# Performance work log

Hardware: AMD Instinct MI355X
Metric: run time of the kernel (lower is better)

## Reference

```python
import jax, jax.numpy as jnp
import numpy as np
import math

NUM_HEADS = 8
WINDOW = 8  # stage=1


def _windowed_attention(q, kv, Wq, bq, Wk, bk, Wv, bv, Wo, bo):
    B, N, C = q.shape
    H = W = int(math.isqrt(N))
    nh, ws = NUM_HEADS, WINDOW
    hd = C // nh
    scale = hd ** -0.5

    qp = q @ Wq + bq   # (B, N, C)
    kp = kv @ Wk + bk
    vp = kv @ Wv + bv

    def to_windows(x):
        # (B, N, C) -> (B, nh, nWh*nWw, ws*ws, hd)
        x = x.reshape(B, H // ws, ws, W // ws, ws, nh, hd)
        x = x.transpose(0, 5, 1, 3, 2, 4, 6)  # B, nh, nWh, nWw, ws, ws, hd
        return x.reshape(B, nh, (H // ws) * (W // ws), ws * ws, hd)

    qw = to_windows(qp)
    kw = to_windows(kp)
    vw = to_windows(vp)

    attn = jnp.einsum('bhnqd,bhnkd->bhnqk', qw, kw) * scale
    attn = jax.nn.softmax(attn.astype(jnp.float32), axis=-1).astype(qw.dtype)
    ow = jnp.einsum('bhnqk,bhnkd->bhnqd', attn, vw)

    # window reverse: (B, nh, nW, ws*ws, hd) -> (B, N, C)
    ow = ow.reshape(B, nh, H // ws, W // ws, ws, ws, hd)
    ow = ow.transpose(0, 2, 4, 3, 5, 1, 6)  # B, nWh, ws, nWw, ws, nh, hd
    x = ow.reshape(B, N, C)

    return x @ Wo + bo


def setup_inputs() -> dict:
    key = jax.random.key(0)
    ks = jax.random.split(key, 7)
    B, N, C = 4, 16384, 256
    s = 1.0 / math.sqrt(C)
    return {
        'q': jax.random.normal(ks[0], (B, N, C), jnp.float32),
        'kv': jax.random.normal(ks[1], (B, N, C), jnp.float32),
        'Wq': jax.random.normal(ks[2], (C, C), jnp.float32) * s,
        'bq': jnp.zeros((C,), jnp.float32),
        'Wk': jax.random.normal(ks[3], (C, C), jnp.float32) * s,
        'bk': jnp.zeros((C,), jnp.float32),
        'Wv': jax.random.normal(ks[4], (C, C), jnp.float32) * s,
        'bv': jnp.zeros((C,), jnp.float32),
        'Wo': jax.random.normal(ks[5], (C, C), jnp.float32) * s,
        'bo': jnp.zeros((C,), jnp.float32),
    }


def reference(q, kv, Wq, bq, Wk, bk, Wv, bv, Wo, bo):
    return _windowed_attention(q, kv, Wq, bq, Wk, bk, Wv, bv, Wo, bo)
```

## Files before the change

kernel.cpp:

```cpp
#include <hip/hip_runtime.h>
#include <hip/hip_bf16.h>

typedef __bf16 bf16;
typedef __bf16 bf16x8 __attribute__((ext_vector_type(8)));
typedef float  f32x4  __attribute__((ext_vector_type(4)));

#define DEVINL __device__ __forceinline__

DEVINL void gll16(const void* g, void* l) {
  __builtin_amdgcn_global_load_lds(
      (const __attribute__((address_space(1))) unsigned int*)g,
      (__attribute__((address_space(3))) unsigned int*)l, 16, 0, 0);
}

__global__ void k_prep(const float* __restrict__ Wq, const float* __restrict__ Wk,
                       const float* __restrict__ Wv, const float* __restrict__ Wo,
                       bf16* __restrict__ packQ, bf16* __restrict__ packO) {
  const int n = threadIdx.x;
  const int k = blockIdx.x;
  const int m = blockIdx.y;
  const int kk = k & 63, iter4 = k >> 6;
  const int h = kk >> 5, kg = (kk >> 3) & 3, e = k & 7;
  if (m < 3) {
    const float* W = (m == 0) ? Wq : (m == 1) ? Wk : Wv;
    const bf16 v = (bf16)W[k * 256 + n];
    const int nglob = m * 256 + n;
    const int tile = nglob >> 7, row = nglob & 127;
    packQ[(size_t)((tile * 4 + iter4) * 1024 + h * 512 + row * 4 + kg) * 8 + e] = v;
  } else {
    const float w = Wo[k * 256 + n];
    const bf16 hi = (bf16)w;
    const bf16 v = (m == 3) ? hi : (bf16)(w - (float)hi);
    const int iter = (m - 3) * 4 + iter4;
    const int tile = n >> 7, row = n & 127;
    packO[(size_t)((tile * 8 + iter) * 1024 + h * 512 + row * 4 + kg) * 8 + e] = v;
  }
}

__global__ __launch_bounds__(256, 3) void k_qkv(
    const float* __restrict__ q, const float* __restrict__ kv,
    const bf16* __restrict__ packQ,
    const float* __restrict__ bq, const float* __restrict__ bk,
    const float* __restrict__ bvv,
    bf16* __restrict__ qp, bf16* __restrict__ kp, bf16* __restrict__ vp) {
  __shared__ __align__(16) bf16 As[2][128 * 32];
  __shared__ __align__(16) bf16 Bs[2][128 * 32];

  const int g = blockIdx.x, xcd = g & 7, s = g >> 3;
  const int nb = s % 6, mh = s / 6;
  const int m0 = (mh * 8 + xcd) * 128;
  const float* A = (nb < 2) ? q : kv;

  const int tid = threadIdx.x, lane = tid & 63, wave = tid >> 6;
  const int mw = (wave >> 1) * 64, nw = (wave & 1) * 64;
  const int lm = lane & 15, lq = lane >> 4;

  f32x4 acc[4][4];
#pragma unroll
  for (int a = 0; a < 4; ++a)
#pragma unroll
    for (int b = 0; b < 4; ++b) acc[a][b] = (f32x4)0.0f;

  const int rowA = tid >> 1;
  const int hA = tid & 1;
  const bf16* pbase = packQ + (size_t)nb * 4 * 8192;

  for (int i = 0; i < 4; ++i) {
    const bf16* pit = pbase + i * 8192;
#pragma unroll
    for (int u = 0; u < 4; ++u) {
      const int c = u * 256 + tid;
      bf16* dst = (u < 2) ? &Bs[0][c * 8] : &Bs[1][(c - 512) * 8];
      gll16(pit + c * 8, dst);
    }
    const float* srcA = A + (size_t)(m0 + rowA) * 256 + i * 64 + hA * 32;
    bf16* dstA = &As[hA][rowA * 32];
#pragma unroll
    for (int half = 0; half < 2; ++half) {
      const float4 f0 = *(const float4*)(srcA + half * 16 + 0);
      const float4 f1 = *(const float4*)(srcA + half * 16 + 4);
      const float4 f2 = *(const float4*)(srcA + half * 16 + 8);
      const float4 f3 = *(const float4*)(srcA + half * 16 + 12);
      bf16x8 b0, b1;
      b0[0] = (bf16)f0.x; b0[1] = (bf16)f0.y; b0[2] = (bf16)f0.z; b0[3] = (bf16)f0.w;
      b0[4] = (bf16)f1.x; b0[5] = (bf16)f1.y; b0[6] = (bf16)f1.z; b0[7] = (bf16)f1.w;
      b1[0] = (bf16)f2.x; b1[1] = (bf16)f2.y; b1[2] = (bf16)f2.z; b1[3] = (bf16)f2.w;
      b1[4] = (bf16)f3.x; b1[5] = (bf16)f3.y; b1[6] = (bf16)f3.z; b1[7] = (bf16)f3.w;
      *(bf16x8*)&dstA[half * 16] = b0;
      *(bf16x8*)&dstA[half * 16 + 8] = b1;
    }
    __syncthreads();
#pragma unroll
    for (int ks = 0; ks < 2; ++ks) {
      bf16x8 av[4], bvf[4];
#pragma unroll
      for (int t = 0; t < 4; ++t)
        av[t] = *(const bf16x8*)&As[ks][(mw + t * 16 + lm) * 32 + lq * 8];
#pragma unroll
      for (int t = 0; t < 4; ++t)
        bvf[t] = *(const bf16x8*)&Bs[ks][(nw + t * 16 + lm) * 32 + lq * 8];
#pragma unroll
      for (int a = 0; a < 4; ++a)
#pragma unroll
        for (int b = 0; b < 4; ++b)
          acc[a][b] = __builtin_amdgcn_mfma_f32_16x16x32_bf16(av[a], bvf[b], acc[a][b], 0, 0, 0);
    }
    __syncthreads();
  }

#pragma unroll
  for (int a = 0; a < 4; ++a)
#pragma unroll
    for (int b = 0; b < 4; ++b) {
      const int nglob = nb * 128 + nw + b * 16 + lm;
      bf16* op; const float* bp; int nc;
      if (nglob < 256)      { op = qp; nc = nglob;       bp = bq; }
      else if (nglob < 512) { op = kp; nc = nglob - 256; bp = bk; }
      else                  { op = vp; nc = nglob - 512; bp = bvv; }
      const float bval = bp[nc];
#pragma unroll
      for (int r = 0; r < 4; ++r) {
        const int mg = m0 + mw + a * 16 + lq * 4 + r;
        op[(size_t)mg * 256 + nc] = (bf16)(acc[a][b][r] + bval);
      }
    }
}

__global__ __launch_bounds__(256, 3) void k_oproj(
    const bf16* __restrict__ ao, const bf16* __restrict__ packO,
    const float* __restrict__ bo, float* __restrict__ out) {
  __shared__ __align__(16) bf16 As[2][128 * 32];
  __shared__ __align__(16) bf16 Bs[2][128 * 32];

  const int g = blockIdx.x, xcd = g & 7, s = g >> 3;
  const int nb = s & 1, mh = s >> 1;
  const int m0 = (mh * 8 + xcd) * 128;

  const int tid = threadIdx.x, lane = tid & 63, wave = tid >> 6;
  const int mw = (wave >> 1) * 64, nw = (wave & 1) * 64;
  const int lm = lane & 15, lq = lane >> 4;

  f32x4 acc[4][4];
#pragma unroll
  for (int a = 0; a < 4; ++a)
#pragma unroll
    for (int b = 0; b < 4; ++b) acc[a][b] = (f32x4)0.0f;

  const bf16* pbase = packO + (size_t)nb * 8 * 8192;

  for (int i = 0; i < 8; ++i) {
    const int kA = (i & 3) * 64;
#pragma unroll
    for (int u = 0; u < 4; ++u) {
      const int c = u * 256 + tid;
      const int h = c >> 9, r2 = c & 511;
      const int row = r2 >> 2, kg = c & 3;
      bf16* dstB = (u < 2) ? &Bs[0][c * 8] : &Bs[1][(c - 512) * 8];
      gll16(pbase + (size_t)i * 8192 + c * 8, dstB);
      bf16* dstA = (u < 2) ? &As[0][r2 * 8] : &As[1][r2 * 8];
      gll16(ao + (size_t)(m0 + row) * 256 + kA + h * 32 + kg * 8, dstA);
    }
    __syncthreads();
#pragma unroll
    for (int ks = 0; ks < 2; ++ks) {
      bf16x8 av[4], bvf[4];
#pragma unroll
      for (int t = 0; t < 4; ++t)
        av[t] = *(const bf16x8*)&As[ks][(mw + t * 16 + lm) * 32 + lq * 8];
#pragma unroll
      for (int t = 0; t < 4; ++t)
        bvf[t] = *(const bf16x8*)&Bs[ks][(nw + t * 16 + lm) * 32 + lq * 8];
#pragma unroll
      for (int a = 0; a < 4; ++a)
#pragma unroll
        for (int b = 0; b < 4; ++b)
          acc[a][b] = __builtin_amdgcn_mfma_f32_16x16x32_bf16(av[a], bvf[b], acc[a][b], 0, 0, 0);
    }
    __syncthreads();
  }

#pragma unroll
  for (int a = 0; a < 4; ++a)
#pragma unroll
    for (int b = 0; b < 4; ++b) {
      const int nglob = nb * 128 + nw + b * 16 + lm;
      const float bval = bo[nglob];
#pragma unroll
      for (int r = 0; r < 4; ++r) {
        const int mg = m0 + mw + a * 16 + lq * 4 + r;
        out[(size_t)mg * 256 + nglob] = acc[a][b][r] + bval;
      }
    }
}

__global__ __launch_bounds__(256) void k_attn(
    const bf16* __restrict__ qp, const bf16* __restrict__ kp,
    const bf16* __restrict__ vp, bf16* __restrict__ ao) {
  __shared__ __align__(16) bf16 smem[3 * 64 * 136];
  bf16* Qs = smem;
  bf16* Ks = smem + 64 * 136;
  bf16* Vs = smem + 2 * 64 * 136;
  bf16* Ps = smem;
  bf16* Os = Vs;

  const int tid = threadIdx.x;
  const int lane = tid & 63;
  const int hl = tid >> 6;
  const int bw = blockIdx.x;
  const int b = bw >> 8;
  const int w = bw & 255;
  const int wy = w >> 4, wx = w & 15;
  const int ch0 = blockIdx.y * 128;

#pragma unroll
  for (int i = 0; i < 4; ++i) {
    const int c = i * 256 + tid;
    const int t = c >> 4;
    const int off = (c & 15) * 8;
    const int ty = t >> 3, tx = t & 7;
    const size_t gr = ((size_t)(b * 128 + wy * 8 + ty)) * 128 + wx * 8 + tx;
    const size_t gi = gr * 256 + ch0 + off;
    const int li = t * 136 + off;
    *(uint4*)&Qs[li] = *(const uint4*)&qp[gi];
    *(uint4*)&Ks[li] = *(const uint4*)&kp[gi];
    *(uint4*)&Vs[li] = *(const uint4*)&vp[gi];
  }
  __syncthreads();

  const int chh = hl * 32;
  const int lm = lane & 15;
  const int lq = lane >> 4;

  bf16x8 qa[4], kb[4];
#pragma unroll
  for (int t = 0; t < 4; ++t)
    qa[t] = *(const bf16x8*)&Qs[(t * 16 + lm) * 136 + chh + lq * 8];
#pragma unroll
  for (int t = 0; t < 4; ++t)
    kb[t] = *(const bf16x8*)&Ks[(t * 16 + lm) * 136 + chh + lq * 8];

  f32x4 s[4][4];
#pragma unroll
  for (int i = 0; i < 4; ++i)
#pragma unroll
    for (int j = 0; j < 4; ++j) s[i][j] = (f32x4)0.0f;
#pragma unroll
  for (int i = 0; i < 4; ++i)
#pragma unroll
    for (int j = 0; j < 4; ++j)
      s[i][j] = __builtin_amdgcn_mfma_f32_16x16x32_bf16(qa[i], kb[j], s[i][j], 0, 0, 0);

  const float scale = 0.17677669529663687f;
  float rl[4][4];
#pragma unroll
  for (int mt = 0; mt < 4; ++mt) {
#pragma unroll
    for (int r = 0; r < 4; ++r) {
      float mx = fmaxf(fmaxf(s[mt][0][r], s[mt][1][r]), fmaxf(s[mt][2][r], s[mt][3][r]));
      mx = fmaxf(mx, __shfl_xor(mx, 1));
      mx = fmaxf(mx, __shfl_xor(mx, 2));
      mx = fmaxf(mx, __shfl_xor(mx, 4));
      mx = fmaxf(mx, __shfl_xor(mx, 8));
      float sum = 0.f;
#pragma unroll
      for (int nt = 0; nt < 4; ++nt) {
        const float p = __expf((s[mt][nt][r] - mx) * scale);
        s[mt][nt][r] = p;
        sum += p;
      }
      sum += __shfl_xor(sum, 1);
      sum += __shfl_xor(sum, 2);
      sum += __shfl_xor(sum, 4);
      sum += __shfl_xor(sum, 8);
      rl[mt][r] = 1.0f / sum;
    }
  }

  __syncthreads();

  bf16* Ph = Ps + hl * 4096;
#pragma unroll
  for (int mt = 0; mt < 4; ++mt)
#pragma unroll
    for (int nt = 0; nt < 4; ++nt)
#pragma unroll
      for (int r = 0; r < 4; ++r) {
        const int qrow = mt * 16 + lq * 4 + r;
        const int kcol = nt * 16 + lm;
        Ph[qrow * 64 + (((kcol >> 3) ^ (qrow & 7)) << 3) + (kcol & 7)] = (bf16)s[mt][nt][r];
      }

  f32x4 o[4][2];
#pragma unroll
  for (int i = 0; i < 4; ++i) { o[i][0] = (f32x4)0.0f; o[i][1] = (f32x4)0.0f; }
#pragma unroll
  for (int ks = 0; ks < 2; ++ks) {
    bf16x8 pa[4];
#pragma unroll
    for (int mt = 0; mt < 4; ++mt) {
      const int qrow = mt * 16 + lm;
      const int gsel = ks * 4 + lq;
      pa[mt] = *(const bf16x8*)&Ph[qrow * 64 + ((gsel ^ (qrow & 7)) << 3)];
    }
    bf16x8 vbf[2];
#pragma unroll
    for (int ntd = 0; ntd < 2; ++ntd) {
      const int d = ntd * 16 + lm;
      bf16x8 tv;
#pragma unroll
      for (int j = 0; j < 8; ++j)
        tv[j] = Vs[(ks * 32 + lq * 8 + j) * 136 + chh + d];
      vbf[ntd] = tv;
    }
#pragma unroll
    for (int mt = 0; mt < 4; ++mt)
#pragma unroll
      for (int ntd = 0; ntd < 2; ++ntd)
        o[mt][ntd] = __builtin_amdgcn_mfma_f32_16x16x32_bf16(pa[mt], vbf[ntd], o[mt][ntd], 0, 0, 0);
  }

  __syncthreads();

#pragma unroll
  for (int mt = 0; mt < 4; ++mt)
#pragma unroll
    for (int ntd = 0; ntd < 2; ++ntd)
#pragma unroll
      for (int r = 0; r < 4; ++r) {
        const int qrow = mt * 16 + lq * 4 + r;
        const int d = ntd * 16 + lm;
        Os[qrow * 136 + chh + d] = (bf16)(o[mt][ntd][r] * rl[mt][r]);
      }
  __syncthreads();

#pragma unroll
  for (int i = 0; i < 4; ++i) {
    const int c = i * 256 + tid;
    const int t = c >> 4;
    const int off = (c & 15) * 8;
    const int ty = t >> 3, tx = t & 7;
    const size_t gr = ((size_t)(b * 128 + wy * 8 + ty)) * 128 + wx * 8 + tx;
    *(uint4*)&ao[gr * 256 + ch0 + off] = *(const uint4*)&Os[t * 136 + off];
  }
}

extern "C" void kernel_launch(void* const* d_in, const int* in_sizes, int n_in,
                              void* d_out, int out_size, void* d_ws, size_t ws_size,
                              hipStream_t stream) {
  const float* q  = (const float*)d_in[0];
  const float* kv = (const float*)d_in[1];
  const float* Wq = (const float*)d_in[2];
  const float* bq = (const float*)d_in[3];
  const float* Wk = (const float*)d_in[4];
  const float* bk = (const float*)d_in[5];
  const float* Wv = (const float*)d_in[6];
  const float* bv = (const float*)d_in[7];
  const float* Wo = (const float*)d_in[8];
  const float* bo = (const float*)d_in[9];
  float* out = (float*)d_out;

  char* ws = (char*)d_ws;
  bf16* packQ = (bf16*)(ws + 0);
  bf16* packO = (bf16*)(ws + 393216);
  const size_t PLANE = (size_t)65536 * 256 * 2;
  bf16* qp = (bf16*)(ws + 1048576);
  bf16* kp = (bf16*)(ws + 1048576 + PLANE);
  bf16* vp = (bf16*)(ws + 1048576 + 2 * PLANE);
  bf16* ao = (bf16*)(ws + 1048576 + 3 * PLANE);
  if (ws_size < 1048576 + 4 * PLANE) return;

  k_prep<<<dim3(256, 5), 256, 0, stream>>>(Wq, Wk, Wv, Wo, packQ, packO);
  k_qkv<<<3072, 256, 0, stream>>>(q, kv, packQ, bq, bk, bv, qp, kp, vp);
  k_attn<<<dim3(1024, 2), 256, 0, stream>>>(qp, kp, vp, ao);
  k_oproj<<<1024, 256, 0, stream>>>(ao, packO, bo, out);
}
```

Before: 302.1 us.

## Double-buffer QKV GEMM B tiles, load A directly into registers, swizzle LDS

The QKV projection kernel now reads the fp32 activation rows straight from global memory into registers, converts them to bf16 there and feeds them to MFMA, so the A tile no longer goes through LDS. The weight tiles are double-buffered in LDS with prefetch of the next iteration, which drops one barrier per iteration. The packed weight layout gets an XOR swizzle on the k-group to reduce LDS bank conflicts. Wave tiling changes from 2x2 (64x64) to 4x1 (32x128). The cost is more accumulator and prefetch registers, and each wave reads the weight tile separately.

Result: faster. 296.2 us (-2.0%).

```diff
diff --git a/kernel.cpp b/kernel.cpp
--- a/kernel.cpp
+++ b/kernel.cpp
@@ -26,7 +26,8 @@
     const bf16 v = (bf16)W[k * 256 + n];
     const int nglob = m * 256 + n;
     const int tile = nglob >> 7, row = nglob & 127;
-    packQ[(size_t)((tile * 4 + iter4) * 1024 + h * 512 + row * 4 + kg) * 8 + e] = v;
+    const int kgs = kg ^ ((row >> 1) & 3);
+    packQ[(size_t)((tile * 4 + iter4) * 1024 + h * 512 + row * 4 + kgs) * 8 + e] = v;
   } else {
     const float w = Wo[k * 256 + n];
     const bf16 hi = (bf16)w;
@@ -43,8 +44,7 @@
     const float* __restrict__ bq, const float* __restrict__ bk,
     const float* __restrict__ bvv,
     bf16* __restrict__ qp, bf16* __restrict__ kp, bf16* __restrict__ vp) {
-  __shared__ __align__(16) bf16 As[2][128 * 32];
-  __shared__ __align__(16) bf16 Bs[2][128 * 32];
+  __shared__ __align__(16) bf16 Bs[2][2][128 * 32];
 
   const int g = blockIdx.x, xcd = g & 7, s = g >> 3;
   const int nb = s % 6, mh = s / 6;
@@ -52,76 +52,92 @@
   const float* A = (nb < 2) ? q : kv;
 
   const int tid = threadIdx.x, lane = tid & 63, wave = tid >> 6;
-  const int mw = (wave >> 1) * 64, nw = (wave & 1) * 64;
   const int lm = lane & 15, lq = lane >> 4;
-
-  f32x4 acc[4][4];
-#pragma unroll
-  for (int a = 0; a < 4; ++a)
-#pragma unroll
-    for (int b = 0; b < 4; ++b) acc[a][b] = (f32x4)0.0f;
-
-  const int rowA = tid >> 1;
-  const int hA = tid & 1;
+  const int swzlq = lq ^ ((lm >> 1) & 3);
+  const int mw = wave * 32;
+
+  f32x4 acc[2][8];
+#pragma unroll
+  for (int t = 0; t < 2; ++t)
+#pragma unroll
+    for (int nf = 0; nf < 8; ++nf) acc[t][nf] = (f32x4)0.0f;
+
   const bf16* pbase = packQ + (size_t)nb * 4 * 8192;
-
-  for (int i = 0; i < 4; ++i) {
-    const bf16* pit = pbase + i * 8192;
+  const float* arow0 = A + (size_t)(m0 + mw + lm) * 256 + lq * 8;
+  const float* arow1 = arow0 + (size_t)16 * 256;
+
+  float4 ar[2][2][2];
+
+  auto stageB = [&](int it, int buf) {
+    const bf16* pit = pbase + it * 8192;
 #pragma unroll
     for (int u = 0; u < 4; ++u) {
       const int c = u * 256 + tid;
-      bf16* dst = (u < 2) ? &Bs[0][c * 8] : &Bs[1][(c - 512) * 8];
+      bf16* dst = (u < 2) ? &Bs[buf][0][c * 8] : &Bs[buf][1][(c - 512) * 8];
       gll16(pit + c * 8, dst);
     }
-    const float* srcA = A + (size_t)(m0 + rowA) * 256 + i * 64 + hA * 32;
-    bf16* dstA = &As[hA][rowA * 32];
-#pragma unroll
-    for (int half = 0; half < 2; ++half) {
-      const float4 f0 = *(const float4*)(srcA + half * 16 + 0);
-      const float4 f1 = *(const float4*)(srcA + half * 16 + 4);
-      const float4 f2 = *(const float4*)(srcA + half * 16 + 8);
-      const float4 f3 = *(const float4*)(srcA + half * 16 + 12);
-      bf16x8 b0, b1;
-      b0[0] = (bf16)f0.x; b0[1] = (bf16)f0.y; b0[2] = (bf16)f0.z; b0[3] = (bf16)f0.w;
-      b0[4] = (bf16)f1.x; b0[5] = (bf16)f1.y; b0[6] = (bf16)f1.z; b0[7] = (bf16)f1.w;
-      b1[0] = (bf16)f2.x; b1[1] = (bf16)f2.y; b1[2] = (bf16)f2.z; b1[3] = (bf16)f2.w;
-      b1[4] = (bf16)f3.x; b1[5] = (bf16)f3.y; b1[6] = (bf16)f3.z; b1[7] = (bf16)f3.w;
-      *(bf16x8*)&dstA[half * 16] = b0;
-      *(bf16x8*)&dstA[half * 16 + 8] = b1;
-    }
-    __syncthreads();
+  };
+  auto loadA = [&](int it) {
+#pragma unroll
+    for (int t = 0; t < 2; ++t)
+#pragma unroll
+      for (int ks = 0; ks < 2; ++ks) {
+        const float* p = (t == 0 ? arow0 : arow1) + it * 64 + ks * 32;
+        ar[t][ks][0] = *(const float4*)(p);
+        ar[t][ks][1] = *(const float4*)(p + 4);
+      }
+  };
+
+  stageB(0, 0);
+  loadA(0);
+  __syncthreads();
+
+#pragma unroll
+  for (int i = 0; i < 4; ++i) {
+    const int cur = i & 1;
+    if (i < 3) stageB(i + 1, cur ^ 1);
+
+    bf16x8 av[2][2];
+#pragma unroll
+    for (int t = 0; t < 2; ++t)
+#pragma unroll
+      for (int ks = 0; ks < 2; ++ks) {
+        const float4 f0 = ar[t][ks][0], f1 = ar[t][ks][1];
+        bf16x8 v;
+        v[0] = (bf16)f0.x; v[1] = (bf16)f0.y; v[2] = (bf16)f0.z; v[3] = (bf16)f0.w;
+        v[4] = (bf16)f1.x; v[5] = (bf16)f1.y; v[6] = (bf16)f1.z; v[7] = (bf16)f1.w;
+        av[t][ks] = v;
+      }
+    if (i < 3) loadA(i + 1);
+
 #pragma unroll
     for (int ks = 0; ks < 2; ++ks) {
-      bf16x8 av[4], bvf[4];
-#pragma unroll
-      for (int t = 0; t < 4; ++t)
-        av[t] = *(const bf16x8*)&As[ks][(mw + t * 16 + lm) * 32 + lq * 8];
-#pragma unroll
-      for (int t = 0; t < 4; ++t)
-        bvf[t] = *(const bf16x8*)&Bs[ks][(nw + t * 16 + lm) * 32 + lq * 8];
-#pragma unroll
-      for (int a = 0; a < 4; ++a)
-#pragma unroll
-        for (int b = 0; b < 4; ++b)
-          acc[a][b] = __builtin_amdgcn_mfma_f32_16x16x32_bf16(av[a], bvf[b], acc[a][b], 0, 0, 0);
-    }
-    __syncthreads();
-  }
-
-#pragma unroll
-  for (int a = 0; a < 4; ++a)
-#pragma unroll
-    for (int b = 0; b < 4; ++b) {
-      const int nglob = nb * 128 + nw + b * 16 + lm;
-      bf16* op; const float* bp; int nc;
-      if (nglob < 256)      { op = qp; nc = nglob;       bp = bq; }
-      else if (nglob < 512) { op = kp; nc = nglob - 256; bp = bk; }
-      else                  { op = vp; nc = nglob - 512; bp = bvv; }
+      bf16x8 bvf[8];
+#pragma unroll
+      for (int nf = 0; nf < 8; ++nf)
+        bvf[nf] = *(const bf16x8*)&Bs[cur][ks][(nf * 16 + lm) * 32 + swzlq * 8];
+#pragma unroll
+      for (int t = 0; t < 2; ++t)
+#pragma unroll
+        for (int nf = 0; nf < 8; ++nf)
+          acc[t][nf] = __builtin_amdgcn_mfma_f32_16x16x32_bf16(av[t][ks], bvf[nf], acc[t][nf], 0, 0, 0);
+    }
+    if (i < 3) __syncthreads();
+  }
+
+  const int ncbase = (nb * 128) & 255;
+  bf16* op = (nb < 2) ? qp : (nb < 4) ? kp : vp;
+  const float* bp = (nb < 2) ? bq : (nb < 4) ? bk : bvv;
+#pragma unroll
+  for (int t = 0; t < 2; ++t)
+#pragma unroll
+    for (int nf = 0; nf < 8; ++nf) {
+      const int nc = ncbase + nf * 16 + lm;
       const float bval = bp[nc];
 #pragma unroll
       for (int r = 0; r < 4; ++r) {
-        const int mg = m0 + mw + a * 16 + lq * 4 + r;
-        op[(size_t)mg * 256 + nc] = (bf16)(acc[a][b][r] + bval);
+        const int mg = m0 + mw + t * 16 + lq * 4 + r;
+        op[(size_t)mg * 256 + nc] = (bf16)(acc[t][nf][r] + bval);
       }
     }
 }
```

## Fuse QKV projection, windowed attention and output projection into one per-window kernel

Applied to the files above, without the earlier changes.

Replaces the three kernels (QKV GEMM, windowed attention, output GEMM) with a single kernel. Each 256-thread block handles one 8x8 window: it loads q and kv for the window into swizzled LDS, projects Q/K/V with weights read straight from global memory in an MFMA-fragment-packed layout, runs softmax attention for 8 heads, then applies the output projection and writes fp32 output. This removes the bf16 qp/kp/vp/ao intermediates that made round trips through HBM, plus two launches. In exchange it uses about 96KB of LDS per block, so occupancy is limited to one block per CU, and every block re-reads the weight matrices from cache.

Measured after the change: 294.8 us. 2.4% less time.

```diff
diff --git a/kernel.cpp b/kernel.cpp
--- a/kernel.cpp
+++ b/kernel.cpp
@@ -3,344 +3,266 @@
 
 typedef __bf16 bf16;
 typedef __bf16 bf16x8 __attribute__((ext_vector_type(8)));
+typedef __bf16 bf16x4 __attribute__((ext_vector_type(4)));
 typedef float  f32x4  __attribute__((ext_vector_type(4)));
 
-#define DEVINL __device__ __forceinline__
-
-DEVINL void gll16(const void* g, void* l) {
-  __builtin_amdgcn_global_load_lds(
-      (const __attribute__((address_space(1))) unsigned int*)g,
-      (__attribute__((address_space(3))) unsigned int*)l, 16, 0, 0);
-}
+#define MFMA __builtin_amdgcn_mfma_f32_16x16x32_bf16
 
 __global__ void k_prep(const float* __restrict__ Wq, const float* __restrict__ Wk,
                        const float* __restrict__ Wv, const float* __restrict__ Wo,
-                       bf16* __restrict__ packQ, bf16* __restrict__ packO) {
+                       bf16* __restrict__ packW, bf16* __restrict__ packO) {
   const int n = threadIdx.x;
   const int k = blockIdx.x;
   const int m = blockIdx.y;
-  const int kk = k & 63, iter4 = k >> 6;
-  const int h = kk >> 5, kg = (kk >> 3) & 3, e = k & 7;
+  const int nsl = n >> 6, nf = (n >> 4) & 3, lm = n & 15;
+  const int ks = k >> 5, lq = (k >> 3) & 3, e = k & 7;
   if (m < 3) {
     const float* W = (m == 0) ? Wq : (m == 1) ? Wk : Wv;
     const bf16 v = (bf16)W[k * 256 + n];
-    const int nglob = m * 256 + n;
-    const int tile = nglob >> 7, row = nglob & 127;
-    packQ[(size_t)((tile * 4 + iter4) * 1024 + h * 512 + row * 4 + kg) * 8 + e] = v;
+    const size_t slot = ((size_t)(m * 4 + nsl) * 8 + ks) * 4 + nf;
+    packW[slot * 512 + (lq * 16 + lm) * 8 + e] = v;
   } else {
-    const float w = Wo[k * 256 + n];
-    const bf16 hi = (bf16)w;
-    const bf16 v = (m == 3) ? hi : (bf16)(w - (float)hi);
-    const int iter = (m - 3) * 4 + iter4;
-    const int tile = n >> 7, row = n & 127;
-    packO[(size_t)((tile * 8 + iter) * 1024 + h * 512 + row * 4 + kg) * 8 + e] = v;
+    const float wv = Wo[k * 256 + n];
+    const bf16 hi = (bf16)wv;
+    const bf16 v = (m == 3) ? hi : (bf16)(wv - (float)hi);
+    const int kss = (m == 3) ? ks : 8 + ks;
+    const size_t slot = ((size_t)nsl * 16 + kss) * 4 + nf;
+    packO[slot * 512 + (lq * 16 + lm) * 8 + e] = v;
   }
 }
 
-__global__ __launch_bounds__(256, 3) void k_qkv(
+__global__ __launch_bounds__(256, 1) void k_fused(
     const float* __restrict__ q, const float* __restrict__ kv,
-    const bf16* __restrict__ packQ,
+    const bf16* __restrict__ packW, const bf16* __restrict__ packO,
     const float* __restrict__ bq, const float* __restrict__ bk,
-    const float* __restrict__ bvv,
-    bf16* __restrict__ qp, bf16* __restrict__ kp, bf16* __restrict__ vp) {
-  __shared__ __align__(16) bf16 As[2][128 * 32];
-  __shared__ __align__(16) bf16 Bs[2][128 * 32];
-
-  const int g = blockIdx.x, xcd = g & 7, s = g >> 3;
-  const int nb = s % 6, mh = s / 6;
-  const int m0 = (mh * 8 + xcd) * 128;
-  const float* A = (nb < 2) ? q : kv;
+    const float* __restrict__ bvv, const float* __restrict__ bo,
+    float* __restrict__ out) {
+  __shared__ __align__(16) bf16 bufA[64 * 256];
+  __shared__ __align__(16) bf16 bufB[64 * 256];
+  __shared__ __align__(16) bf16 bufC[64 * 256];
 
   const int tid = threadIdx.x, lane = tid & 63, wave = tid >> 6;
-  const int mw = (wave >> 1) * 64, nw = (wave & 1) * 64;
   const int lm = lane & 15, lq = lane >> 4;
-
-  f32x4 acc[4][4];
-#pragma unroll
-  for (int a = 0; a < 4; ++a)
-#pragma unroll
-    for (int b = 0; b < 4; ++b) acc[a][b] = (f32x4)0.0f;
-
-  const int rowA = tid >> 1;
-  const int hA = tid & 1;
-  const bf16* pbase = packQ + (size_t)nb * 4 * 8192;
-
-  for (int i = 0; i < 4; ++i) {
-    const bf16* pit = pbase + i * 8192;
-#pragma unroll
-    for (int u = 0; u < 4; ++u) {
-      const int c = u * 256 + tid;
-      bf16* dst = (u < 2) ? &Bs[0][c * 8] : &Bs[1][(c - 512) * 8];
-      gll16(pit + c * 8, dst);
-    }
-    const float* srcA = A + (size_t)(m0 + rowA) * 256 + i * 64 + hA * 32;
-    bf16* dstA = &As[hA][rowA * 32];
-#pragma unroll
-    for (int half = 0; half < 2; ++half) {
-      const float4 f0 = *(const float4*)(srcA + half * 16 + 0);
-      const float4 f1 = *(const float4*)(srcA + half * 16 + 4);
-      const float4 f2 = *(const float4*)(srcA + half * 16 + 8);
-      const float4 f3 = *(const float4*)(srcA + half * 16 + 12);
-      bf16x8 b0, b1;
-      b0[0] = (bf16)f0.x; b0[1] = (bf16)f0.y; b0[2] = (bf16)f0.z; b0[3] = (bf16)f0.w;
-      b0[4] = (bf16)f1.x; b0[5] = (bf16)f1.y; b0[6] = (bf16)f1.z; b0[7] = (bf16)f1.w;
-      b1[0] = (bf16)f2.x; b1[1] = (bf16)f2.y; b1[2] = (bf16)f2.z; b1[3] = (bf16)f2.w;
-      b1[4] = (bf16)f3.x; b1[5] = (bf16)f3.y; b1[6] = (bf16)f3.z; b1[7] = (bf16)f3.w;
-      *(bf16x8*)&dstA[half * 16] = b0;
-      *(bf16x8*)&dstA[half * 16 + 8] = b1;
-    }
+  const int bw = blockIdx.x, b = bw >> 8, w = bw & 255;
+  const int wy = w >> 4, wx = w & 15;
+  const size_t rowbase = ((size_t)(b * 128 + wy * 8)) * 128 + wx * 8;
+
+  {
+    const int gx = lane >> 1, half = lane & 1;
+#pragma unroll
+    for (int i = 0; i < 16; ++i) {
+      const int tok = i * 4 + wave;
+      const size_t gaddr = (rowbase + (tok >> 3) * 128 + (tok & 7)) * 256 + lane * 4;
+      const int la = tok * 256 + ((gx ^ (tok & 7)) << 3) + half * 4;
+      float4 f = *(const float4*)(q + gaddr);
+      bf16x4 v;
+      v[0] = (bf16)f.x; v[1] = (bf16)f.y; v[2] = (bf16)f.z; v[3] = (bf16)f.w;
+      *(bf16x4*)&bufA[la] = v;
+      f = *(const float4*)(kv + gaddr);
+      v[0] = (bf16)f.x; v[1] = (bf16)f.y; v[2] = (bf16)f.z; v[3] = (bf16)f.w;
+      *(bf16x4*)&bufB[la] = v;
+    }
+  }
+  __syncthreads();
+
+  auto projAcc = [&](const bf16* Ximg, const bf16* pw, f32x4 (&acc)[4][4]) {
+#pragma unroll
+    for (int nf = 0; nf < 4; ++nf)
+#pragma unroll
+      for (int mf = 0; mf < 4; ++mf) acc[nf][mf] = (f32x4)0.0f;
+#pragma unroll
+    for (int ks = 0; ks < 8; ++ks) {
+      bf16x8 wf[4], xf[4];
+#pragma unroll
+      for (int nf = 0; nf < 4; ++nf)
+        wf[nf] = *(const bf16x8*)(pw + ((size_t)(ks * 4 + nf) * 64 + lane) * 8);
+#pragma unroll
+      for (int mf = 0; mf < 4; ++mf) {
+        const int row = mf * 16 + lm;
+        xf[mf] = *(const bf16x8*)&Ximg[row * 256 + (((ks * 4 + lq) ^ (row & 7)) << 3)];
+      }
+#pragma unroll
+      for (int nf = 0; nf < 4; ++nf)
+#pragma unroll
+        for (int mf = 0; mf < 4; ++mf)
+          acc[nf][mf] = MFMA(wf[nf], xf[mf], acc[nf][mf], 0, 0, 0);
+    }
+  };
+  auto writeProj = [&](bf16* img, const float* bias, f32x4 (&acc)[4][4]) {
+#pragma unroll
+    for (int nf = 0; nf < 4; ++nf) {
+      const int n0 = wave * 64 + nf * 16 + lq * 4;
+      const float4 bb = *(const float4*)(bias + n0);
+      const int gsl = wave * 8 + nf * 2 + (lq >> 1);
+#pragma unroll
+      for (int mf = 0; mf < 4; ++mf) {
+        const int m = mf * 16 + lm;
+        bf16x4 v;
+        v[0] = (bf16)(acc[nf][mf][0] + bb.x);
+        v[1] = (bf16)(acc[nf][mf][1] + bb.y);
+        v[2] = (bf16)(acc[nf][mf][2] + bb.z);
+        v[3] = (bf16)(acc[nf][mf][3] + bb.w);
+        *(bf16x4*)&img[m * 256 + ((gsl ^ (m & 7)) << 3) + (lq & 1) * 4] = v;
+      }
+    }
+  };
+
+  {
+    f32x4 pacc[4][4];
+    projAcc(bufA, packW + (size_t)(0 * 4 + wave) * 16384, pacc);
     __syncthreads();
-#pragma unroll
-    for (int ks = 0; ks < 2; ++ks) {
-      bf16x8 av[4], bvf[4];
-#pragma unroll
-      for (int t = 0; t < 4; ++t)
-        av[t] = *(const bf16x8*)&As[ks][(mw + t * 16 + lm) * 32 + lq * 8];
-#pragma unroll
-      for (int t = 0; t < 4; ++t)
-        bvf[t] = *(const bf16x8*)&Bs[ks][(nw + t * 16 + lm) * 32 + lq * 8];
-#pragma unroll
-      for (int a = 0; a < 4; ++a)
-#pragma unroll
-        for (int b = 0; b < 4; ++b)
-          acc[a][b] = __builtin_amdgcn_mfma_f32_16x16x32_bf16(av[a], bvf[b], acc[a][b], 0, 0, 0);
-    }
+    writeProj(bufA, bq, pacc);
+    projAcc(bufB, packW + (size_t)(1 * 4 + wave) * 16384, pacc);
+    writeProj(bufC, bk, pacc);
+    projAcc(bufB, packW + (size_t)(2 * 4 + wave) * 16384, pacc);
     __syncthreads();
-  }
-
-#pragma unroll
-  for (int a = 0; a < 4; ++a)
-#pragma unroll
-    for (int b = 0; b < 4; ++b) {
-      const int nglob = nb * 128 + nw + b * 16 + lm;
-      bf16* op; const float* bp; int nc;
-      if (nglob < 256)      { op = qp; nc = nglob;       bp = bq; }
-      else if (nglob < 512) { op = kp; nc = nglob - 256; bp = bk; }
-      else                  { op = vp; nc = nglob - 512; bp = bvv; }
-      const float bval = bp[nc];
+    writeProj(bufB, bvv, pacc);
+  }
+
+  const float scale = 0.17677669529663687f;
+  f32x4 s[2][4][4];
+#pragma unroll
+  for (int h = 0; h < 2; ++h) {
+    const int h4 = wave * 8 + h * 4;
+    bf16x8 qa[4], kb[4];
+#pragma unroll
+    for (int t = 0; t < 4; ++t) {
+      const int row = t * 16 + lm;
+      const int go = ((h4 + lq) ^ (row & 7)) << 3;
+      qa[t] = *(const bf16x8*)&bufA[row * 256 + go];
+      kb[t] = *(const bf16x8*)&bufC[row * 256 + go];
+    }
+#pragma unroll
+    for (int i = 0; i < 4; ++i)
+#pragma unroll
+      for (int j = 0; j < 4; ++j) {
+        s[h][i][j] = (f32x4)0.0f;
+        s[h][i][j] = MFMA(qa[i], kb[j], s[h][i][j], 0, 0, 0);
+      }
+  }
+
+#pragma unroll
+  for (int h = 0; h < 2; ++h) {
+    float rl[4][4];
+#pragma unroll
+    for (int mt = 0; mt < 4; ++mt)
 #pragma unroll
       for (int r = 0; r < 4; ++r) {
-        const int mg = m0 + mw + a * 16 + lq * 4 + r;
-        op[(size_t)mg * 256 + nc] = (bf16)(acc[a][b][r] + bval);
-      }
-    }
-}
-
-__global__ __launch_bounds__(256, 3) void k_oproj(
-    const bf16* __restrict__ ao, const bf16* __restrict__ packO,
-    const float* __restrict__ bo, float* __restrict__ out) {
-  __shared__ __align__(16) bf16 As[2][128 * 32];
-  __shared__ __align__(16) bf16 Bs[2][128 * 32];
-
-  const int g = blockIdx.x, xcd = g & 7, s = g >> 3;
-  const int nb = s & 1, mh = s >> 1;
-  const int m0 = (mh * 8 + xcd) * 128;
-
-  const int tid = threadIdx.x, lane = tid & 63, wave = tid >> 6;
-  const int mw = (wave >> 1) * 64, nw = (wave & 1) * 64;
-  const int lm = lane & 15, lq = lane >> 4;
-
-  f32x4 acc[4][4];
-#pragma unroll
-  for (int a = 0; a < 4; ++a)
-#pragma unroll
-    for (int b = 0; b < 4; ++b) acc[a][b] = (f32x4)0.0f;
-
-  const bf16* pbase = packO + (size_t)nb * 8 * 8192;
-
-  for (int i = 0; i < 8; ++i) {
-    const int kA = (i & 3) * 64;
-#pragma unroll
-    for (int u = 0; u < 4; ++u) {
-      const int c = u * 256 + tid;
-      const int h = c >> 9, r2 = c & 511;
-      const int row = r2 >> 2, kg = c & 3;
-      bf16* dstB = (u < 2) ? &Bs[0][c * 8] : &Bs[1][(c - 512) * 8];
-      gll16(pbase + (size_t)i * 8192 + c * 8, dstB);
-      bf16* dstA = (u < 2) ? &As[0][r2 * 8] : &As[1][r2 * 8];
-      gll16(ao + (size_t)(m0 + row) * 256 + kA + h * 32 + kg * 8, dstA);
-    }
-    __syncthreads();
-#pragma unroll
-    for (int ks = 0; ks < 2; ++ks) {
-      bf16x8 av[4], bvf[4];
-#pragma unroll
-      for (int t = 0; t < 4; ++t)
-        av[t] = *(const bf16x8*)&As[ks][(mw + t * 16 + lm) * 32 + lq * 8];
-#pragma unroll
-      for (int t = 0; t < 4; ++t)
-        bvf[t] = *(const bf16x8*)&Bs[ks][(nw + t * 16 + lm) * 32 + lq * 8];
-#pragma unroll
-      for (int a = 0; a < 4; ++a)
-#pragma unroll
-        for (int b = 0; b < 4; ++b)
-          acc[a][b] = __builtin_amdgcn_mfma_f32_16x16x32_bf16(av[a], bvf[b], acc[a][b], 0, 0, 0);
-    }
-    __syncthreads();
-  }
-
-#pragma unroll
-  for (int a = 0; a < 4; ++a)
-#pragma unroll
-    for (int b = 0; b < 4; ++b) {
-      const int nglob = nb * 128 + nw + b * 16 + lm;
-      const float bval = bo[nglob];
-#pragma unroll
-      for (int r = 0; r < 4; ++r) {
-        const int mg = m0 + mw + a * 16 + lq * 4 + r;
-        out[(size_t)mg * 256 + nglob] = acc[a][b][r] + bval;
-      }
-    }
-}
-
-__global__ __launch_bounds__(256) void k_attn(
-    const bf16* __restrict__ qp, const bf16* __restrict__ kp,
-    const bf16* __restrict__ vp, bf16* __restrict__ ao) {
-  __shared__ __align__(16) bf16 smem[3 * 64 * 136];
-  bf16* Qs = smem;
-  bf16* Ks = smem + 64 * 136;
-  bf16* Vs = smem + 2 * 64 * 136;
-  bf16* Ps = smem;
-  bf16* Os = Vs;
-
-  const int tid = threadIdx.x;
-  const int lane = tid & 63;
-  const int hl = tid >> 6;
-  const int bw = blockIdx.x;
-  const int b = bw >> 8;
-  const int w = bw & 255;
-  const int wy = w >> 4, wx = w & 15;
-  const int ch0 = blockIdx.y * 128;
-
-#pragma unroll
-  for (int i = 0; i < 4; ++i) {
-    const int c = i * 256 + tid;
-    const int t = c >> 4;
-    const int off = (c & 15) * 8;
-    const int ty = t >> 3, tx = t & 7;
-    const size_t gr = ((size_t)(b * 128 + wy * 8 + ty)) * 128 + wx * 8 + tx;
-    const size_t gi = gr * 256 + ch0 + off;
-    const int li = t * 136 + off;
-    *(uint4*)&Qs[li] = *(const uint4*)&qp[gi];
-    *(uint4*)&Ks[li] = *(const uint4*)&kp[gi];
-    *(uint4*)&Vs[li] = *(const uint4*)&vp[gi];
+        float mx = fmaxf(fmaxf(s[h][mt][0][r], s[h][mt][1][r]),
+                         fmaxf(s[h][mt][2][r], s[h][mt][3][r]));
+        mx = fmaxf(mx, __shfl_xor(mx, 1));
+        mx = fmaxf(mx, __shfl_xor(mx, 2));
+        mx = fmaxf(mx, __shfl_xor(mx, 4));
+        mx = fmaxf(mx, __shfl_xor(mx, 8));
+        float sum = 0.f;
+#pragma unroll
+        for (int nt = 0; nt < 4; ++nt) {
+          const float p = __expf((s[h][mt][nt][r] - mx) * scale);
+          s[h][mt][nt][r] = p;
+          sum += p;
+        }
+        sum += __shfl_xor(sum, 1);
+        sum += __shfl_xor(sum, 2);
+        sum += __shfl_xor(sum, 4);
+        sum += __shfl_xor(sum, 8);
+        rl[mt][r] = 1.0f / sum;
+      }
+
+#pragma unroll
+    for (int mt = 0; mt < 4; ++mt)
+#pragma unroll
+      for (int nt = 0; nt < 4; ++nt)
+#pragma unroll
+        for (int r = 0; r < 4; ++r) {
+          const int qrow = mt * 16 + lq * 4 + r;
+          const int kcol = nt * 16 + lm;
+          bufC[qrow * 256 + ((wave * 8 + ((kcol >> 3) ^ (qrow & 7))) << 3) + (kcol & 7)] =
+              (bf16)s[h][mt][nt][r];
+        }
+
+    f32x4 o[4][2];
+#pragma unroll
+    for (int i = 0; i < 4; ++i) { o[i][0] = (f32x4)0.0f; o[i][1] = (f32x4)0.0f; }
+#pragma unroll
+    for (int ks2 = 0; ks2 < 2; ++ks2) {
+      bf16x8 pa[4];
+#pragma unroll
+      for (int mt = 0; mt < 4; ++mt) {
+        const int qrow = mt * 16 + lm;
+        const int gsel = ks2 * 4 + lq;
+        pa[mt] = *(const bf16x8*)&bufC[qrow * 256 + ((wave * 8 + (gsel ^ (qrow & 7))) << 3)];
+      }
+      bf16x8 vb[2];
+#pragma unroll
+      for (int ntd = 0; ntd < 2; ++ntd) {
+        const int gv = wave * 8 + h * 4 + ntd * 2 + (lm >> 3);
+        bf16x8 tv;
+#pragma unroll
+        for (int j = 0; j < 8; ++j) {
+          const int tok = ks2 * 32 + lq * 8 + j;
+          tv[j] = bufB[tok * 256 + ((gv ^ (tok & 7)) << 3) + (lm & 7)];
+        }
+        vb[ntd] = tv;
+      }
+#pragma unroll
+      for (int mt = 0; mt < 4; ++mt)
+#pragma unroll
+        for (int ntd = 0; ntd < 2; ++ntd)
+          o[mt][ntd] = MFMA(pa[mt], vb[ntd], o[mt][ntd], 0, 0, 0);
+    }
+
+#pragma unroll
+    for (int mt = 0; mt < 4; ++mt)
+#pragma unroll
+      for (int ntd = 0; ntd < 2; ++ntd) {
+        const int gv = wave * 8 + h * 4 + ntd * 2 + (lm >> 3);
+#pragma unroll
+        for (int r = 0; r < 4; ++r) {
+          const int tok = mt * 16 + lq * 4 + r;
+          bufA[tok * 256 + ((gv ^ (tok & 7)) << 3) + (lm & 7)] =
+              (bf16)(o[mt][ntd][r] * rl[mt][r]);
+        }
+      }
   }
   __syncthreads();
 
-  const int chh = hl * 32;
-  const int lm = lane & 15;
-  const int lq = lane >> 4;
-
-  bf16x8 qa[4], kb[4];
-#pragma unroll
-  for (int t = 0; t < 4; ++t)
-    qa[t] = *(const bf16x8*)&Qs[(t * 16 + lm) * 136 + chh + lq * 8];
-#pragma unroll
-  for (int t = 0; t < 4; ++t)
-    kb[t] = *(const bf16x8*)&Ks[(t * 16 + lm) * 136 + chh + lq * 8];
-
-  f32x4 s[4][4];
-#pragma unroll
-  for (int i = 0; i < 4; ++i)
-#pragma unroll
-    for (int j = 0; j < 4; ++j) s[i][j] = (f32x4)0.0f;
-#pragma unroll
-  for (int i = 0; i < 4; ++i)
-#pragma unroll
-    for (int j = 0; j < 4; ++j)
-      s[i][j] = __builtin_amdgcn_mfma_f32_16x16x32_bf16(qa[i], kb[j], s[i][j], 0, 0, 0);
-
-  const float scale = 0.17677669529663687f;
-  float rl[4][4];
-#pragma unroll
-  for (int mt = 0; mt < 4; ++mt) {
-#pragma unroll
-    for (int r = 0; r < 4; ++r) {
-      float mx = fmaxf(fmaxf(s[mt][0][r], s[mt][1][r]), fmaxf(s[mt][2][r], s[mt][3][r]));
-      mx = fmaxf(mx, __shfl_xor(mx, 1));
-      mx = fmaxf(mx, __shfl_xor(mx, 2));
-      mx = fmaxf(mx, __shfl_xor(mx, 4));
-      mx = fmaxf(mx, __shfl_xor(mx, 8));
-      float sum = 0.f;
-#pragma unroll
-      for (int nt = 0; nt < 4; ++nt) {
-        const float p = __expf((s[mt][nt][r] - mx) * scale);
-        s[mt][nt][r] = p;
-        sum += p;
-      }
-      sum += __shfl_xor(sum, 1);
-      sum += __shfl_xor(sum, 2);
-      sum += __shfl_xor(sum, 4);
-      sum += __shfl_xor(sum, 8);
-      rl[mt][r] = 1.0f / sum;
-    }
-  }
-
-  __syncthreads();
-
-  bf16* Ph = Ps + hl * 4096;
-#pragma unroll
-  for (int mt = 0; mt < 4; ++mt)
-#pragma unroll
-    for (int nt = 0; nt < 4; ++nt)
-#pragma unroll
-      for (int r = 0; r < 4; ++r) {
-        const int qrow = mt * 16 + lq * 4 + r;
-        const int kcol = nt * 16 + lm;
-        Ph[qrow * 64 + (((kcol >> 3) ^ (qrow & 7)) << 3) + (kcol & 7)] = (bf16)s[mt][nt][r];
-      }
-
-  f32x4 o[4][2];
-#pragma unroll
-  for (int i = 0; i < 4; ++i) { o[i][0] = (f32x4)0.0f; o[i][1] = (f32x4)0.0f; }
-#pragma unroll
-  for (int ks = 0; ks < 2; ++ks) {
-    bf16x8 pa[4];
-#pragma unroll
-    for (int mt = 0; mt < 4; ++mt) {
-      const int qrow = mt * 16 + lm;
-      const int gsel = ks * 4 + lq;
-      pa[mt] = *(const bf16x8*)&Ph[qrow * 64 + ((gsel ^ (qrow & 7)) << 3)];
-    }
-    bf16x8 vbf[2];
-#pragma unroll
-    for (int ntd = 0; ntd < 2; ++ntd) {
-      const int d = ntd * 16 + lm;
-      bf16x8 tv;
-#pragma unroll
-      for (int j = 0; j < 8; ++j)
-        tv[j] = Vs[(ks * 32 + lq * 8 + j) * 136 + chh + d];
-      vbf[ntd] = tv;
-    }
-#pragma unroll
-    for (int mt = 0; mt < 4; ++mt)
-#pragma unroll
-      for (int ntd = 0; ntd < 2; ++ntd)
-        o[mt][ntd] = __builtin_amdgcn_mfma_f32_16x16x32_bf16(pa[mt], vbf[ntd], o[mt][ntd], 0, 0, 0);
-  }
-
-  __syncthreads();
-
-#pragma unroll
-  for (int mt = 0; mt < 4; ++mt)
-#pragma unroll
-    for (int ntd = 0; ntd < 2; ++ntd)
-#pragma unroll
-      for (int r = 0; r < 4; ++r) {
-        const int qrow = mt * 16 + lq * 4 + r;
-        const int d = ntd * 16 + lm;
-        Os[qrow * 136 + chh + d] = (bf16)(o[mt][ntd][r] * rl[mt][r]);
-      }
-  __syncthreads();
-
-#pragma unroll
-  for (int i = 0; i < 4; ++i) {
-    const int c = i * 256 + tid;
-    const int t = c >> 4;
-    const int off = (c & 15) * 8;
-    const int ty = t >> 3, tx = t & 7;
-    const size_t gr = ((size_t)(b * 128 + wy * 8 + ty)) * 128 + wx * 8 + tx;
-    *(uint4*)&ao[gr * 256 + ch0 + off] = *(const uint4*)&Os[t * 136 + off];
+  {
+    f32x4 oacc[4][4];
+#pragma unroll
+    for (int mf = 0; mf < 4; ++mf)
+#pragma unroll
+      for (int nf = 0; nf < 4; ++nf) oacc[mf][nf] = (f32x4)0.0f;
+    const bf16* po = packO + (size_t)wave * 32768;
+#pragma unroll
+    for (int ks = 0; ks < 16; ++ks) {
+      bf16x8 af[4], bf_[4];
+#pragma unroll
+      for (int mf = 0; mf < 4; ++mf) {
+        const int row = mf * 16 + lm;
+        af[mf] = *(const bf16x8*)&bufA[row * 256 + ((((ks & 7) * 4 + lq) ^ (row & 7)) << 3)];
+      }
+#pragma unroll
+      for (int nf = 0; nf < 4; ++nf)
+        bf_[nf] = *(const bf16x8*)(po + ((size_t)(ks * 4 + nf) * 64 + lane) * 8);
+#pragma unroll
+      for (int mf = 0; mf < 4; ++mf)
+#pragma unroll
+        for (int nf = 0; nf < 4; ++nf)
+          oacc[mf][nf] = MFMA(af[mf], bf_[nf], oacc[mf][nf], 0, 0, 0);
+    }
+#pragma unroll
+    for (int nf = 0; nf < 4; ++nf) {
+      const int n = wave * 64 + nf * 16 + lm;
+      const float bval = bo[n];
+#pragma unroll
+      for (int mf = 0; mf < 4; ++mf)
+#pragma unroll
+        for (int r = 0; r < 4; ++r) {
+          const int tok = mf * 16 + lq * 4 + r;
+          const size_t gr = rowbase + (tok >> 3) * 128 + (tok & 7);
+          out[gr * 256 + n] = oacc[mf][nf][r] + bval;
+        }
+    }
   }
 }
 
@@ -360,17 +282,10 @@
   float* out = (float*)d_out;
 
   char* ws = (char*)d_ws;
-  bf16* packQ = (bf16*)(ws + 0);
+  bf16* packW = (bf16*)(ws + 0);
   bf16* packO = (bf16*)(ws + 393216);
-  const size_t PLANE = (size_t)65536 * 256 * 2;
-  bf16* qp = (bf16*)(ws + 1048576);
-  bf16* kp = (bf16*)(ws + 1048576 + PLANE);
-  bf16* vp = (bf16*)(ws + 1048576 + 2 * PLANE);
-  bf16* ao = (bf16*)(ws + 1048576 + 3 * PLANE);
-  if (ws_size < 1048576 + 4 * PLANE) return;
-
-  k_prep<<<dim3(256, 5), 256, 0, stream>>>(Wq, Wk, Wv, Wo, packQ, packO);
-  k_qkv<<<3072, 256, 0, stream>>>(q, kv, packQ, bq, bk, bv, qp, kp, vp);
-  k_attn<<<dim3(1024, 2), 256, 0, stream>>>(qp, kp, vp, ao);
-  k_oproj<<<1024, 256, 0, stream>>>(ao, packO, bo, out);
+  if (ws_size < 655360) return;
+
+  k_prep<<<dim3(256, 5), 256, 0, stream>>>(Wq, Wk, Wv, Wo, packW, packO);
+  k_fused<<<1024, 256, 0, stream>>>(q, kv, packW, packO, bq, bk, bv, bo, out);
 }
```
